# Kernel tuning notes

Measured on AMD Instinct MI355X. Metric: run time of the kernel, lower is better.

## Reference

```python
import jax, jax.numpy as jnp
import numpy as np

B, T, H, IN = 256, 1024, 512, 1

def setup_inputs() -> dict:
    key = jax.random.key(0)
    ks = jax.random.split(key, 10)
    s = 1.0 / np.sqrt(H)
    return {
        "input": jax.random.normal(ks[0], (B, T), dtype=jnp.float32),
        "Wx0": jax.random.uniform(ks[1], (IN, 4 * H), jnp.float32, -s, s),
        "Wh0": jax.random.uniform(ks[2], (H, 4 * H), jnp.float32, -s, s),
        "b0": jax.random.uniform(ks[3], (4 * H,), jnp.float32, -s, s),
        "Wx1": jax.random.uniform(ks[4], (H, 4 * H), jnp.float32, -s, s),
        "Wh1": jax.random.uniform(ks[5], (H, 4 * H), jnp.float32, -s, s),
        "b1": jax.random.uniform(ks[6], (4 * H,), jnp.float32, -s, s),
        "Wf": jax.random.uniform(ks[7], (H, 1), jnp.float32, -s, s),
        "bf": jax.random.uniform(ks[8], (1,), jnp.float32, -s, s),
    }

def _lstm_layer(xs, Wx, Wh, b):
    # xs: [T, B, in] -> hs: [T, B, H]
    Bd = xs.shape[1]
    Hd = Wh.shape[0]
    h0 = jnp.zeros((Bd, Hd), xs.dtype)
    c0 = jnp.zeros((Bd, Hd), xs.dtype)
    def step(carry, x_t):
        h, c = carry
        g = x_t @ Wx + h @ Wh + b                     # [B, 4H]
        i, f, gg, o = jnp.split(g, 4, axis=-1)
        i = jax.nn.sigmoid(i)
        f = jax.nn.sigmoid(f)
        gg = jnp.tanh(gg)
        o = jax.nn.sigmoid(o)
        c_n = f * c + i * gg
        h_n = o * jnp.tanh(c_n)
        return (h_n, c_n), h_n
    _, hs = jax.lax.scan(step, (h0, c0), xs)
    return hs

def reference(input, Wx0, Wh0, b0, Wx1, Wh1, b1, Wf, bf):
    # input: [B, T] scalar sequence (input_size = 1)
    xs = input.T[:, :, None]                           # [T, B, 1]
    h1 = _lstm_layer(xs, Wx0, Wh0, b0)                 # [T, B, H]
    h2 = _lstm_layer(h1, Wx1, Wh1, b1)                 # [T, B, H]
    out = h2 @ Wf + bf                                 # [T, B, 1]
    return out[:, :, 0].T                              # [B, T]
```

## Files before the change

kernel.cpp:

```cpp
#include <hip/hip_runtime.h>


typedef _Float16 f16;
typedef _Float16 f16x8 __attribute__((ext_vector_type(8)));
typedef float f32x4 __attribute__((ext_vector_type(4)));
typedef unsigned long long u64;

#define NB 256
#define NT_ 1024
#define NH 512
#define RING 16
#define SLOT (NB * NH)

__device__ __forceinline__ float sigm(float x)  { return 1.0f / (1.0f + __expf(-x)); }
__device__ __forceinline__ float tanhx(float x) { return 2.0f / (1.0f + __expf(-2.0f * x)) - 1.0f; }

__device__ __forceinline__ void st8(unsigned short* p, u64 v) {
  __hip_atomic_store((u64*)p, v, __ATOMIC_RELAXED, __HIP_MEMORY_SCOPE_AGENT);
}
__device__ __forceinline__ void stf(unsigned* p, unsigned v) {
  __hip_atomic_store(p, v, __ATOMIC_RELAXED, __HIP_MEMORY_SCOPE_AGENT);
}
__device__ __forceinline__ unsigned ldf(const unsigned* p) {
  return __hip_atomic_load(p, __ATOMIC_RELAXED, __HIP_MEMORY_SCOPE_AGENT);
}
__device__ __forceinline__ unsigned pollr(const unsigned* a, unsigned thr) {
  unsigned v;
  for (;;) {
    v = ldf(a);
    if (!~__ballot(v >= thr)) break;
    __builtin_amdgcn_s_sleep(1);
  }
  asm volatile("" ::: "memory");
  return v;
}

__global__ void prep_xT(const float* __restrict__ inp, float* __restrict__ xT) {
  int g = blockIdx.x * 256 + threadIdx.x;
  int t = g >> 8, b = g & 255;
  xT[t * NB + b] = inp[b * NT_ + t];
}

__global__ void prep_w(const float* __restrict__ Wh0,
                       const float* __restrict__ Wx1,
                       const float* __restrict__ Wh1,
                       f16* __restrict__ dst) {
  int g = blockIdx.x * 256 + threadIdx.x;
  int mat = g >> 20;
  int r = g & 0xFFFFF;
  int j = r & 7, ln = (r >> 3) & 63, kt = (r >> 9) & 15;
  int cl = ln & 15, qd = ln >> 4;
  int k = kt * 32 + qd * 8 + j;
  size_t di; int gcol; const float* W;
  if (mat == 0) {
    int gt = (r >> 13) & 3, nh = (r >> 15) & 1, sl = (r >> 16) & 15;
    W = Wh0;
    gcol = gt * 512 + sl * 32 + nh * 16 + cl;
    di = (size_t)sl * 65536 + (((size_t)(nh * 4 + gt) * 16 + kt) * 64 + ln) * 8 + j;
  } else {
    int jt = (r >> 13) & 1, nh = (r >> 14) & 1, sl = (r >> 15) & 31;
    W = (mat == 1) ? Wx1 : Wh1;
    int gate = jt * 2 + (cl >> 3);
    gcol = gate * 512 + sl * 16 + nh * 8 + (cl & 7);
    di = (size_t)mat * 1048576 + (size_t)sl * 32768 +
         (((size_t)(nh * 2 + jt) * 16 + kt) * 64 + ln) * 8 + j;
  }
  dst[di] = (f16)W[(size_t)k * 2048 + gcol];
}

__global__ void reduce_out(const float* __restrict__ part8,
                           const float* __restrict__ bfp,
                           float* __restrict__ out) {
  int g = blockIdx.x * 256 + threadIdx.x;
  float v = bfp[0];
#pragma unroll
  for (int j = 0; j < 8; ++j) v += part8[(size_t)j * (NB * NT_) + g];
  out[g] = v;
}

__global__ __launch_bounds__(256, 1) void lstm_main(
    const float* __restrict__ xT,
    const f16*  __restrict__ wsl,
    const float* __restrict__ wx0,
    const float* __restrict__ bias0,
    const float* __restrict__ bias1,
    const float* __restrict__ wf,
    unsigned short* p_hi, unsigned short* p_lo,
    unsigned short* q_hi, unsigned short* q_lo,
    unsigned int* pf,
    unsigned int* qf,
    float* part8)
{
  extern __shared__ char smem[];
  const int tid = threadIdx.x;
  const int wv = tid >> 6, ln = tid & 63;
  const int qd = ln >> 4, cl = ln & 15;
  const int bx = blockIdx.x;
  const int r8 = bx & 7, idx = bx >> 3;
  const bool isL0 = !(r8 & 1);
  const int c = r8 >> 1;
  const int sl = idx;
  if (isL0 && idx >= 16) return;
  const float LO = 1.0f / 1024.0f;

  if (isL0) {
    const int4* s0 = (const int4*)wsl + (size_t)sl * 8192;
    int4* d = (int4*)smem;
    for (int i = tid; i < 8192; i += 256) d[i] = s0[i];
  } else {
    const int4* s1 = (const int4*)wsl + 131072 + (size_t)sl * 4096;
    const int4* s2 = (const int4*)wsl + 262144 + (size_t)sl * 4096;
    int4* d = (int4*)smem;
    for (int i = tid; i < 4096; i += 256) { d[i] = s1[i]; d[4096 + i] = s2[i]; }
  }
  __syncthreads();

  unsigned* pfc = pf + (sl & 3) * 128 + c * 32;
  unsigned* qfc = qf + (sl & 3) * 128 + c * 32;

  if (isL0) {
    const int nh = wv >> 1, rhalf = wv & 1;
    const int rb0 = c * 64 + rhalf * 32;
    float wx0v[4], b0c[4];
#pragma unroll
    for (int g = 0; g < 4; ++g) {
      int gc = g * 512 + sl * 32 + nh * 16 + cl;
      wx0v[g] = wx0[gc];
      b0c[g] = bias0[gc];
    }
    float cst[2][4] = {{0.f,0.f,0.f,0.f},{0.f,0.f,0.f,0.f}};
    const bool isq = (ln >= 16 && ln < 48);
    const unsigned* pwa = isq ? (qfc + (ln & 31)) : (pfc + (ln & 15));
    const f16x8* wl = (const f16x8*)smem;
    f16* sh  = (f16*)(smem + 131072);
    f16* slo = sh + 2048;

    for (int s = 0; s < NT_; ++s) {
      if ((s & (RING - 1)) == 0 && s) {
        __syncthreads();
        if (wv == 0)
          asm volatile("buffer_inv sc1\n\ts_waitcnt vmcnt(0)" ::: "memory");
        __syncthreads();
      }
      const int slot_r = (s + RING - 1) & (RING - 1);
      const int slot_w = s & (RING - 1);
      float4 xv[2];
#pragma unroll
      for (int rt = 0; rt < 2; ++rt)
        xv[rt] = *(const float4*)(xT + s * NB + rb0 + rt * 16 + qd * 4);
      if (s) {
        unsigned thr = isq ? (s >= RING ? (unsigned)(s - RING + 1) : 0u)
                           : (unsigned)s;
        if (wv == 0) pollr(pwa, thr);
        __syncthreads();
      }
      f16x8 Ah[16][2], Al[16][2];
      {
        const f16* bh = (const f16*)p_hi + (size_t)slot_r * SLOT + (size_t)c * 32768 + qd * 8;
        const f16* bl = (const f16*)p_lo + (size_t)slot_r * SLOT + (size_t)c * 32768 + qd * 8;
#pragma unroll
        for (int kt = 0; kt < 16; ++kt)
#pragma unroll
          for (int rt = 0; rt < 2; ++rt) {
            int lr = rhalf * 32 + rt * 16 + cl;
            size_t off = (size_t)kt * 2048 + lr * 32;
            Ah[kt][rt] = *(const f16x8*)(bh + off);
            Al[kt][rt] = *(const f16x8*)(bl + off);
          }
      }
      f32x4 acc[4][2], accL[4][2];
#pragma unroll
      for (int g = 0; g < 4; ++g)
#pragma unroll
        for (int rt = 0; rt < 2; ++rt) {
          acc[g][rt] = (f32x4){0.f,0.f,0.f,0.f};
          accL[g][rt] = (f32x4){0.f,0.f,0.f,0.f};
        }
#pragma unroll
      for (int kt = 0; kt < 16; ++kt) {
#pragma unroll
        for (int g = 0; g < 4; ++g) {
          f16x8 bw = wl[((nh * 4 + g) * 16 + kt) * 64 + ln];
#pragma unroll
          for (int rt = 0; rt < 2; ++rt) {
            acc[g][rt]  = __builtin_amdgcn_mfma_f32_16x16x32_f16(Ah[kt][rt], bw, acc[g][rt], 0, 0, 0);
            accL[g][rt] = __builtin_amdgcn_mfma_f32_16x16x32_f16(Al[kt][rt], bw, accL[g][rt], 0, 0, 0);
          }
        }
      }
#pragma unroll
      for (int rt = 0; rt < 2; ++rt)
#pragma unroll
        for (int e = 0; e < 4; ++e) {
          float xe = (e == 0) ? xv[rt].x : (e == 1) ? xv[rt].y : (e == 2) ? xv[rt].z : xv[rt].w;
          float gi = acc[0][rt][e] + accL[0][rt][e] * LO + xe * wx0v[0] + b0c[0];
          float gf = acc[1][rt][e] + accL[1][rt][e] * LO + xe * wx0v[1] + b0c[1];
          float gg = acc[2][rt][e] + accL[2][rt][e] * LO + xe * wx0v[2] + b0c[2];
          float go = acc[3][rt][e] + accL[3][rt][e] * LO + xe * wx0v[3] + b0c[3];
          float ii = sigm(gi), ff = sigm(gf), tg = tanhx(gg), oo = sigm(go);
          cst[rt][e] = ff * cst[rt][e] + ii * tg;
          float h = oo * tanhx(cst[rt][e]);
          f16 hh = (f16)h;
          int su = (rhalf * 32 + rt * 16 + qd * 4 + e) * 32 + nh * 16 + cl;
          sh[su]  = hh;
          slo[su] = (f16)((h - (float)hh) * 1024.0f);
        }
      __syncthreads();
      {
        unsigned short* bh = p_hi + (size_t)slot_w * SLOT + (size_t)c * 32768 + (size_t)sl * 2048;
        unsigned short* bl = p_lo + (size_t)slot_w * SLOT + (size_t)c * 32768 + (size_t)sl * 2048;
#pragma unroll
        for (int i = tid; i < 1024; i += 256) {
          int strm = i >> 9, pc = i & 511;
          const f16* src = (strm ? slo : sh) + pc * 4;
          st8((strm ? bl : bh) + pc * 4, *(const u64*)src);
        }
      }
      __syncthreads();
      if (tid < 4)
        stf(pf + tid * 128 + c * 32 + sl, (unsigned)(s + 1));
    }
  } else {
    int u = cl & 7, g01 = cl >> 3;
    const bool hiH = (cl < 8);
    float b1c0[2], b1c1[2], wfv[2];
#pragma unroll
    for (int nh = 0; nh < 2; ++nh) {
      int base = sl * 16 + nh * 8 + u;
      b1c0[nh] = bias1[g01 * 512 + base];
      b1c1[nh] = bias1[(2 + g01) * 512 + base];
      wfv[nh] = wf[base];
    }
    const int lr = wv * 16 + cl;
    float cst[2][4] = {{0.f,0.f,0.f,0.f},{0.f,0.f,0.f,0.f}};
    unsigned pf_seen = 0;
    const f16x8* wx_ = (const f16x8*)smem;
    const f16x8* wh_ = (const f16x8*)(smem + 65536);
    f16* sh  = (f16*)(smem + 131072);
    f16* slo = sh + 1024;

    for (int s = 0; s < NT_; ++s) {
      if ((s & (RING - 1)) == 0 && s) {
        __syncthreads();
        if (wv == 0)
          asm volatile("buffer_inv sc1\n\ts_waitcnt vmcnt(0)" ::: "memory");
        __syncthreads();
      }
      const int slot_r = (s + RING - 1) & (RING - 1);
      const int slot_w = s & (RING - 1);
      if (s) {
        if (wv == 0) pollr(qfc + (ln & 31), (unsigned)s);
        __syncthreads();
      }
      const f16* aqh = (const f16*)q_hi + (size_t)slot_r * SLOT + (size_t)c * 32768 +
                       (qd >> 1) * 1024 + lr * 16 + (qd & 1) * 8;
      const f16* aql = (const f16*)q_lo + (size_t)slot_r * SLOT + (size_t)c * 32768 +
                       (qd >> 1) * 1024 + lr * 16 + (qd & 1) * 8;
      f16x8 Aq[16][2];
#pragma unroll
      for (int kt = 0; kt < 16; ++kt) {
        Aq[kt][0] = *(const f16x8*)(aqh + kt * 2048);
        Aq[kt][1] = *(const f16x8*)(aql + kt * 2048);
      }
      const f16* aph = (const f16*)p_hi + (size_t)slot_w * SLOT + (size_t)c * 32768 +
                       lr * 32 + qd * 8;
      const f16* apl = (const f16*)p_lo + (size_t)slot_w * SLOT + (size_t)c * 32768 +
                       lr * 32 + qd * 8;
      bool early = __all((int)(pf_seen >= (unsigned)(s + 1)));
      f16x8 Ap[16][2];
      if (early) {
#pragma unroll
        for (int kt = 0; kt < 16; ++kt) {
          Ap[kt][0] = *(const f16x8*)(aph + kt * 2048);
          Ap[kt][1] = *(const f16x8*)(apl + kt * 2048);
        }
      }
      f32x4 acc[4], accL[4];
#pragma unroll
      for (int t4 = 0; t4 < 4; ++t4) {
        acc[t4] = (f32x4){0.f,0.f,0.f,0.f};
        accL[t4] = (f32x4){0.f,0.f,0.f,0.f};
      }
#pragma unroll
      for (int kt = 0; kt < 16; ++kt) {
#pragma unroll
        for (int t4 = 0; t4 < 4; ++t4) {
          f16x8 bw = wh_[(t4 * 16 + kt) * 64 + ln];
          acc[t4]  = __builtin_amdgcn_mfma_f32_16x16x32_f16(Aq[kt][0], bw, acc[t4], 0, 0, 0);
          accL[t4] = __builtin_amdgcn_mfma_f32_16x16x32_f16(Aq[kt][1], bw, accL[t4], 0, 0, 0);
        }
      }
      if (!early) {
        pf_seen = pollr(pfc + (ln & 15), (unsigned)(s + 1));
#pragma unroll
        for (int kt = 0; kt < 16; ++kt) {
          Ap[kt][0] = *(const f16x8*)(aph + kt * 2048);
          Ap[kt][1] = *(const f16x8*)(apl + kt * 2048);
        }
      }
#pragma unroll
      for (int kt = 0; kt < 16; ++kt) {
#pragma unroll
        for (int t4 = 0; t4 < 4; ++t4) {
          f16x8 bw = wx_[(t4 * 16 + kt) * 64 + ln];
          acc[t4]  = __builtin_amdgcn_mfma_f32_16x16x32_f16(Ap[kt][0], bw, acc[t4], 0, 0, 0);
          accL[t4] = __builtin_amdgcn_mfma_f32_16x16x32_f16(Ap[kt][1], bw, accL[t4], 0, 0, 0);
        }
      }
      float po[4];
#pragma unroll
      for (int e = 0; e < 4; ++e) {
        po[e] = 0.0f;
#pragma unroll
        for (int nh = 0; nh < 2; ++nh) {
          float v0 = acc[nh*2+0][e] + accL[nh*2+0][e] * LO + b1c0[nh];
          float v1 = acc[nh*2+1][e] + accL[nh*2+1][e] * LO + b1c1[nh];
          float w0 = __shfl_xor(v0, 8, 16);
          float w1 = __shfl_xor(v1, 8, 16);
          float gi = hiH ? v0 : w0;
          float gf = hiH ? w0 : v0;
          float gg = hiH ? v1 : w1;
          float go = hiH ? w1 : v1;
          float ii = sigm(gi), ff = sigm(gf), tg = tanhx(gg), oo = sigm(go);
          cst[nh][e] = ff * cst[nh][e] + ii * tg;
          float h = oo * tanhx(cst[nh][e]);
          int su = (wv * 16 + qd * 4 + e) * 16 + nh * 8 + u;
          if (hiH) {
            sh[su] = (f16)h;
          } else {
            f16 hh = (f16)h;
            slo[su] = (f16)((h - (float)hh) * 1024.0f);
          }
          po[e] += hiH ? wfv[nh] * h : 0.0f;
        }
      }
      __syncthreads();
      {
        unsigned short* bhq = q_hi + (size_t)slot_w * SLOT + (size_t)c * 32768 + (size_t)sl * 1024;
        unsigned short* blq = q_lo + (size_t)slot_w * SLOT + (size_t)c * 32768 + (size_t)sl * 1024;
#pragma unroll
        for (int i = tid; i < 512; i += 256) {
          int strm = i >> 8, pc = i & 255;
          const f16* src = (strm ? slo : sh) + pc * 4;
          st8((strm ? blq : bhq) + pc * 4, *(const u64*)src);
        }
      }
      __syncthreads();
      if (tid < 4)
        stf(qf + tid * 128 + c * 32 + sl, (unsigned)(s + 1));
#pragma unroll
      for (int e = 0; e < 4; ++e) {
        float r = po[e];
#pragma unroll
        for (int m = 1; m < 16; m <<= 1) r += __shfl_xor(r, m, 16);
        if (cl == 0)
          atomicAdd(part8 + (size_t)(sl & 7) * (NB * NT_) +
                        (size_t)(c * 64 + wv * 16 + qd * 4 + e) * NT_ + s, r);
      }
    }
  }
}

extern "C" void kernel_launch(void* const* d_in, const int* in_sizes, int n_in,
                              void* d_out, int out_size, void* d_ws, size_t ws_size,
                              hipStream_t stream) {
  (void)in_sizes; (void)n_in; (void)out_size; (void)ws_size;
  const float* inp = (const float*)d_in[0];
  const float* Wx0 = (const float*)d_in[1];
  const float* Wh0 = (const float*)d_in[2];
  const float* b0  = (const float*)d_in[3];
  const float* Wx1 = (const float*)d_in[4];
  const float* Wh1 = (const float*)d_in[5];
  const float* b1  = (const float*)d_in[6];
  const float* Wf  = (const float*)d_in[7];
  const float* bf  = (const float*)d_in[8];

  const size_t MB = 1u << 20;
  const size_t OFF_W    = 0;
  const size_t OFF_XT   = 6 * MB;
  const size_t OFF_PHI  = 7 * MB;
  const size_t OFF_PLO  = 11 * MB;
  const size_t OFF_QHI  = 15 * MB;
  const size_t OFF_QLO  = 19 * MB;
  const size_t OFF_PART = 23 * MB;
  const size_t OFF_CTR  = 31 * MB;

  char* ws = (char*)d_ws;
  f16* wsl = (f16*)(ws + OFF_W);
  float* xT = (float*)(ws + OFF_XT);
  unsigned short* phi = (unsigned short*)(ws + OFF_PHI);
  unsigned short* plo = (unsigned short*)(ws + OFF_PLO);
  unsigned short* qhi = (unsigned short*)(ws + OFF_QHI);
  unsigned short* qlo = (unsigned short*)(ws + OFF_QLO);
  float* part8 = (float*)(ws + OFF_PART);
  unsigned int* pfl = (unsigned int*)(ws + OFF_CTR);
  unsigned int* qfl = pfl + 512;
  float* out = (float*)d_out;

  (void)hipFuncSetAttribute((const void*)lstm_main,
                            hipFuncAttributeMaxDynamicSharedMemorySize, 139264);

  (void)hipMemsetAsync(ws + OFF_PHI, 0, (OFF_CTR + 4096) - OFF_PHI, stream);

  prep_xT<<<1024, 256, 0, stream>>>(inp, xT);
  prep_w<<<12288, 256, 0, stream>>>(Wh0, Wx1, Wh1, wsl);

  lstm_main<<<256, 256, 139264, stream>>>(xT, wsl, Wx0, b0, b1, Wf,
                                          phi, plo, qhi, qlo, pfl, qfl, part8);

  reduce_out<<<1024, 256, 0, stream>>>(part8, bf, out);
}
```

Measured before the change: 10.15 ms.

## Pad step flags to separate cache lines and let every wave poll independently

Each per-block step flag now sits in its own 128-byte slot (stride of 32 uints), with replicas indexed by c, j and r, so producers' writes and pollers' reads do not share cache lines. Every wave now polls its flags itself instead of wave 0 polling followed by a __syncthreads, which removes one barrier per timestep in both layers. Layer 1 folds the early check on the layer-0 flag into the same ballot poll. In exchange the flag area and memset grow, and there are more concurrent polling loads.

```diff
diff --git a/kernel.cpp b/kernel.cpp
--- a/kernel.cpp
+++ b/kernel.cpp
@@ -33,6 +33,13 @@
   }
   asm volatile("" ::: "memory");
   return v;
+}
+
+__device__ __forceinline__ unsigned* PFL(unsigned* pf, int c, int j, int r) {
+  return pf + (((c * 16 + j) * 4) + r) * 32;
+}
+__device__ __forceinline__ unsigned* QFL(unsigned* qf, int c, int j, int r) {
+  return qf + (((c * 32 + j) * 4) + r) * 32;
 }
 
 __global__ void prep_xT(const float* __restrict__ inp, float* __restrict__ xT) {
@@ -115,9 +122,6 @@
   }
   __syncthreads();
 
-  unsigned* pfc = pf + (sl & 3) * 128 + c * 32;
-  unsigned* qfc = qf + (sl & 3) * 128 + c * 32;
-
   if (isL0) {
     const int nh = wv >> 1, rhalf = wv & 1;
     const int rb0 = c * 64 + rhalf * 32;
@@ -130,7 +134,10 @@
     }
     float cst[2][4] = {{0.f,0.f,0.f,0.f},{0.f,0.f,0.f,0.f}};
     const bool isq = (ln >= 16 && ln < 48);
-    const unsigned* pwa = isq ? (qfc + (ln & 31)) : (pfc + (ln & 15));
+    const unsigned* pwa;
+    if (ln < 16)      pwa = PFL(pf, c, ln, sl & 3);
+    else if (ln < 48) pwa = QFL(qf, c, ln - 16, sl & 3);
+    else              pwa = PFL(pf, c, ln - 48, (sl + 1) & 3);
     const f16x8* wl = (const f16x8*)smem;
     f16* sh  = (f16*)(smem + 131072);
     f16* slo = sh + 2048;
@@ -151,8 +158,7 @@
       if (s) {
         unsigned thr = isq ? (s >= RING ? (unsigned)(s - RING + 1) : 0u)
                            : (unsigned)s;
-        if (wv == 0) pollr(pwa, thr);
-        __syncthreads();
+        pollr(pwa, thr);
       }
       f16x8 Ah[16][2], Al[16][2];
       {
@@ -218,7 +224,7 @@
       }
       __syncthreads();
       if (tid < 4)
-        stf(pf + tid * 128 + c * 32 + sl, (unsigned)(s + 1));
+        stf(PFL(pf, c, sl, tid), (unsigned)(s + 1));
     }
   } else {
     int u = cl & 7, g01 = cl >> 3;
@@ -233,7 +239,12 @@
     }
     const int lr = wv * 16 + cl;
     float cst[2][4] = {{0.f,0.f,0.f,0.f},{0.f,0.f,0.f,0.f}};
-    unsigned pf_seen = 0;
+    const unsigned* a_init;
+    const bool isPf = (ln >= 32 && ln < 48);
+    if (ln < 32)      a_init = QFL(qf, c, ln, sl & 3);
+    else if (ln < 48) a_init = PFL(pf, c, ln - 32, sl & 3);
+    else              a_init = QFL(qf, c, ln - 48, (sl + 1) & 3);
+    const unsigned* ppf = PFL(pf, c, ln & 15, (sl + (ln >> 4)) & 3);
     const f16x8* wx_ = (const f16x8*)smem;
     const f16x8* wh_ = (const f16x8*)(smem + 65536);
     f16* sh  = (f16*)(smem + 131072);
@@ -248,9 +259,18 @@
       }
       const int slot_r = (s + RING - 1) & (RING - 1);
       const int slot_w = s & (RING - 1);
+      bool early = false;
       if (s) {
-        if (wv == 0) pollr(qfc + (ln & 31), (unsigned)s);
-        __syncthreads();
+        unsigned thr_i = isPf ? (unsigned)(s + 1) : (unsigned)s;
+        unsigned v = ldf(a_init);
+        u64 bal = __ballot(v >= thr_i);
+        while ((unsigned)bal != 0xFFFFFFFFu) {
+          __builtin_amdgcn_s_sleep(1);
+          v = ldf(a_init);
+          bal = __ballot(v >= thr_i);
+        }
+        asm volatile("" ::: "memory");
+        early = (((bal >> 32) & 0xFFFF) == 0xFFFF);
       }
       const f16* aqh = (const f16*)q_hi + (size_t)slot_r * SLOT + (size_t)c * 32768 +
                        (qd >> 1) * 1024 + lr * 16 + (qd & 1) * 8;
@@ -266,7 +286,6 @@
                        lr * 32 + qd * 8;
       const f16* apl = (const f16*)p_lo + (size_t)slot_w * SLOT + (size_t)c * 32768 +
                        lr * 32 + qd * 8;
-      bool early = __all((int)(pf_seen >= (unsigned)(s + 1)));
       f16x8 Ap[16][2];
       if (early) {
 #pragma unroll
@@ -291,7 +310,7 @@
         }
       }
       if (!early) {
-        pf_seen = pollr(pfc + (ln & 15), (unsigned)(s + 1));
+        pollr(ppf, (unsigned)(s + 1));
 #pragma unroll
         for (int kt = 0; kt < 16; ++kt) {
           Ap[kt][0] = *(const f16x8*)(aph + kt * 2048);
@@ -347,7 +366,7 @@
       }
       __syncthreads();
       if (tid < 4)
-        stf(qf + tid * 128 + c * 32 + sl, (unsigned)(s + 1));
+        stf(QFL(qf, c, sl, tid), (unsigned)(s + 1));
 #pragma unroll
       for (int e = 0; e < 4; ++e) {
         float r = po[e];
@@ -394,13 +413,13 @@
   unsigned short* qlo = (unsigned short*)(ws + OFF_QLO);
   float* part8 = (float*)(ws + OFF_PART);
   unsigned int* pfl = (unsigned int*)(ws + OFF_CTR);
-  unsigned int* qfl = pfl + 512;
+  unsigned int* qfl = pfl + 8192;
   float* out = (float*)d_out;
 
   (void)hipFuncSetAttribute((const void*)lstm_main,
                             hipFuncAttributeMaxDynamicSharedMemorySize, 139264);
 
-  (void)hipMemsetAsync(ws + OFF_PHI, 0, (OFF_CTR + 4096) - OFF_PHI, stream);
+  (void)hipMemsetAsync(ws + OFF_PHI, 0, (OFF_CTR + 98304) - OFF_PHI, stream);
 
   prep_xT<<<1024, 256, 0, stream>>>(inp, xT);
   prep_w<<<12288, 256, 0, stream>>>(Wh0, Wx1, Wh1, wsl);
```

New measurement: 10.21 ms. No clear change (+0.6%).
